# Kernel optimization log

Measured on AMD Instinct MI355X. Metric: run time of the kernel, lower is better.

Reference implementation:

```python
import jax, jax.numpy as jnp
import numpy as np

N, E, F, R = 10000, 320000, 128, 20


def _cross_dim1(a, b):
    # a: [E,3,F], b: [E,3,1]; cross product along axis 1 (broadcast over F)
    return jnp.stack([
        a[:, 1] * b[:, 2] - a[:, 2] * b[:, 1],
        a[:, 2] * b[:, 0] - a[:, 0] * b[:, 2],
        a[:, 0] * b[:, 1] - a[:, 1] * b[:, 0],
    ], axis=1)


def setup_inputs() -> dict:
    key = jax.random.key(0)
    ks = jax.random.split(key, 15)
    s = jax.random.normal(ks[0], (N, F), jnp.float32)
    v = jax.random.normal(ks[1], (N, 3, F), jnp.float32)
    re1 = jax.random.normal(ks[2], (E, R), jnp.float32)
    re2 = jax.random.normal(ks[3], (E, R), jnp.float32)
    f1 = jax.random.uniform(ks[4], (E,), jnp.float32)
    f2 = jax.random.uniform(ks[5], (E,), jnp.float32)
    u1 = jax.random.normal(ks[6], (E, 3), jnp.float32)
    u2 = jax.random.normal(ks[7], (E, 3), jnp.float32)
    edge_index = jax.random.randint(ks[8], (2, E), 0, N, jnp.int32)
    # mlp_phi: Linear(F,F) -> SiLU -> Linear(F,6F); linear_W: Linear(R,6F)
    W1 = jax.random.normal(ks[9], (F, F), jnp.float32) / np.sqrt(F)
    b1 = jnp.zeros((F,), jnp.float32)
    W2 = jax.random.normal(ks[10], (F, 6 * F), jnp.float32) / np.sqrt(F)
    b2 = jnp.zeros((6 * F,), jnp.float32)
    Wr = jax.random.normal(ks[11], (R, 6 * F), jnp.float32) / np.sqrt(R)
    br = jnp.zeros((6 * F,), jnp.float32)
    return dict(s=s, v=v, radial_embeddings_1=re1, radial_embeddings_2=re2,
                f_cut_1=f1, f_cut_2=f2, unit_vectors_1=u1, unit_vectors_2=u2,
                edge_index=edge_index, W1=W1, b1=b1, W2=W2, b2=b2, Wr=Wr, br=br)


def reference(s, v, radial_embeddings_1, radial_embeddings_2, f_cut_1, f_cut_2,
              unit_vectors_1, unit_vectors_2, edge_index, W1, b1, W2, b2, Wr, br):
    idx_i, idx_j = edge_index[0], edge_index[1]
    n_nodes = s.shape[0]
    nf = W1.shape[0]
    # phi: [N, 6F]
    phi = jax.nn.silu(s @ W1 + b1) @ W2 + b2
    # radial gate: [E, 6F]
    W = (radial_embeddings_1 @ Wr + br) * f_cut_1[:, None] \
        + (radial_embeddings_2 @ Wr + br) * f_cut_2[:, None]
    x = phi[idx_j] * W  # [E, 6F]
    x_s, x_vv, x_vs_1, x_vs_2, x_vc_1, x_vc_2 = [
        x[:, i * nf:(i + 1) * nf] for i in range(6)
    ]
    ds = jax.ops.segment_sum(x_s, idx_i, num_segments=n_nodes)  # [N,F]
    v_j = v[idx_j]  # [E,3,F]
    u1 = unit_vectors_1[:, :, None]  # [E,3,1]
    u2 = unit_vectors_2[:, :, None]
    x_v = (v_j * x_vv[:, None, :]
           + x_vs_1[:, None, :] * u1
           + x_vs_2[:, None, :] * u2
           + x_vc_1[:, None, :] * _cross_dim1(v_j, u1)
           + x_vc_2[:, None, :] * _cross_dim1(v_j, u2))  # [E,3,F]
    dv = jax.ops.segment_sum(x_v, idx_i, num_segments=n_nodes)  # [N,3,F]
    return (s + ds, v + dv)
```

## Files before the change

### kernel.cpp

```cpp
#include <hip/hip_runtime.h>
#include <hip/hip_bf16.h>

#define NN   10000
#define NE   320000
#define NF   128
#define SIXF 768
#define K21  21

typedef unsigned short u16;
typedef unsigned int   u32;

__device__ __forceinline__ float bf2f_lo(u32 pk) { return __uint_as_float(pk << 16); }
__device__ __forceinline__ float bf2f_hi(u32 pk) { return __uint_as_float(pk & 0xffff0000u); }
__device__ __forceinline__ u16 f2bf(float f) {
    u32 x = __float_as_uint(f);
    return (u16)((x + 0x7fffu + ((x >> 16) & 1u)) >> 16);
}

__global__ __launch_bounds__(256) void init_out_kernel(
    const float4* __restrict__ s4, const float4* __restrict__ v4, float4* __restrict__ out4)
{
    int i = blockIdx.x * 256 + threadIdx.x;
    if (i < NN * NF / 4) out4[i] = s4[i];
    else                 out4[i] = v4[i - NN * NF / 4];
}

__global__ __launch_bounds__(256) void phi_kernel(
    const float* __restrict__ s, const float* __restrict__ W1, const float* __restrict__ b1,
    const float* __restrict__ W2, const float* __restrict__ b2, u16* __restrict__ phiw)
{
    __shared__ float sh[32][NF];
    __shared__ float hh[32][NF];
    const int t = threadIdx.x;
    const int row0 = blockIdx.x * 32;

    for (int i = t; i < 32 * NF / 4; i += 256) {
        int r = i >> 5, c4 = i & 31;
        float4 val = make_float4(0.f, 0.f, 0.f, 0.f);
        if (row0 + r < NN) val = *reinterpret_cast<const float4*>(&s[(size_t)(row0 + r) * NF + c4 * 4]);
        *reinterpret_cast<float4*>(&sh[r][c4 * 4]) = val;
    }
    __syncthreads();
    {
        const int c = t & 127;
        const int half = t >> 7;
        float hacc[16];
        #pragma unroll
        for (int i = 0; i < 16; ++i) hacc[i] = 0.f;
        for (int k4 = 0; k4 < 32; ++k4) {
            float w0 = W1[(k4 * 4 + 0) * NF + c];
            float w1 = W1[(k4 * 4 + 1) * NF + c];
            float w2 = W1[(k4 * 4 + 2) * NF + c];
            float w3 = W1[(k4 * 4 + 3) * NF + c];
            #pragma unroll
            for (int rr = 0; rr < 16; ++rr) {
                float4 sv = *reinterpret_cast<const float4*>(&sh[half * 16 + rr][k4 * 4]);
                hacc[rr] = fmaf(sv.x, w0, hacc[rr]);
                hacc[rr] = fmaf(sv.y, w1, hacc[rr]);
                hacc[rr] = fmaf(sv.z, w2, hacc[rr]);
                hacc[rr] = fmaf(sv.w, w3, hacc[rr]);
            }
        }
        float b1c = b1[c];
        #pragma unroll
        for (int rr = 0; rr < 16; ++rr) {
            float x = hacc[rr] + b1c;
            float sg = 1.0f / (1.0f + __expf(-x));
            hh[half * 16 + rr][c] = x * sg;
        }
    }
    __syncthreads();
    {
        float pa[32][3];
        #pragma unroll
        for (int r = 0; r < 32; ++r)
            #pragma unroll
            for (int cg = 0; cg < 3; ++cg) pa[r][cg] = 0.f;

        for (int k4 = 0; k4 < 32; ++k4) {
            float w[4][3];
            #pragma unroll
            for (int kk = 0; kk < 4; ++kk)
                #pragma unroll
                for (int cg = 0; cg < 3; ++cg)
                    w[kk][cg] = W2[(size_t)(k4 * 4 + kk) * SIXF + t + 256 * cg];
            #pragma unroll
            for (int r = 0; r < 32; ++r) {
                float4 hv = *reinterpret_cast<const float4*>(&hh[r][k4 * 4]);
                #pragma unroll
                for (int cg = 0; cg < 3; ++cg) {
                    pa[r][cg] = fmaf(hv.x, w[0][cg], pa[r][cg]);
                    pa[r][cg] = fmaf(hv.y, w[1][cg], pa[r][cg]);
                    pa[r][cg] = fmaf(hv.z, w[2][cg], pa[r][cg]);
                    pa[r][cg] = fmaf(hv.w, w[3][cg], pa[r][cg]);
                }
            }
        }
        float b2c[3] = { b2[t], b2[t + 256], b2[t + 512] };
        #pragma unroll
        for (int r = 0; r < 32; ++r) {
            if (row0 + r < NN) {
                #pragma unroll
                for (int cg = 0; cg < 3; ++cg)
                    phiw[(size_t)(row0 + r) * SIXF + t + 256 * cg] = f2bf(pa[r][cg] + b2c[cg]);
            }
        }
    }
}

__global__ __launch_bounds__(256) void prep_wrb_kernel(
    const float* __restrict__ Wr, const float* __restrict__ br, u16* __restrict__ wrb)
{
    int i = blockIdx.x * 256 + threadIdx.x;
    if (i < 21 * SIXF) wrb[i] = f2bf(i < 20 * SIXF ? Wr[i] : br[i - 20 * SIXF]);
}

__global__ __launch_bounds__(256) void prep_vbf_kernel(
    const float* __restrict__ v, u16* __restrict__ vbf)
{
    int i = blockIdx.x * 256 + threadIdx.x;
    if (i < NN * 384) vbf[i] = f2bf(v[i]);
}

__global__ __launch_bounds__(256) void zero_cnt_kernel(int* __restrict__ cnt) {
    int i = blockIdx.x * 256 + threadIdx.x;
    if (i < NN) cnt[i] = 0;
}

__global__ __launch_bounds__(256) void hist_kernel(const int* __restrict__ eidx, int* __restrict__ cnt) {
    int e = blockIdx.x * 256 + threadIdx.x;
    if (e < NE) atomicAdd(&cnt[eidx[e]], 1);
}

__global__ __launch_bounds__(256) void scan_kernel(const int* __restrict__ cnt, int* __restrict__ offs) {
    __shared__ int part[256];
    const int t = threadIdx.x;
    int lsum = 0;
    if (t < 250) {
        #pragma unroll 4
        for (int k = 0; k < 40; ++k) lsum += cnt[t * 40 + k];
    }
    part[t] = lsum;
    __syncthreads();
    if (t == 0) {
        int run = 0;
        for (int i = 0; i < 250; ++i) { int c = part[i]; part[i] = run; run += c; }
    }
    __syncthreads();
    if (t < 250) {
        int run = part[t];
        for (int k = 0; k < 40; ++k) {
            int idx = t * 40 + k;
            offs[idx] = run;
            run += cnt[idx];
        }
    }
}

__global__ __launch_bounds__(256) void scatter_kernel(
    const int* __restrict__ eidx, int* __restrict__ offs, int* __restrict__ elist) {
    int e = blockIdx.x * 256 + threadIdx.x;
    if (e < NE) {
        int pos = atomicAdd(&offs[eidx[e]], 1);
        elist[pos] = e;
    }
}

template<bool USE_VBF>
__global__ __launch_bounds__(256, 4) void gather_kernel(
    const float* __restrict__ re1, const float* __restrict__ re2,
    const float* __restrict__ f1, const float* __restrict__ f2,
    const float* __restrict__ u1v, const float* __restrict__ u2v,
    const int* __restrict__ eidx,
    const u16* __restrict__ phiw, const float* __restrict__ v,
    const u16* __restrict__ vbf, const u16* __restrict__ wrb,
    const float* __restrict__ s,
    const int* __restrict__ cnt, const int* __restrict__ offs,
    const int* __restrict__ elist,
    float* __restrict__ out)
{
    __shared__ u16   WrB[K21][SIXF];
    __shared__ float smem[2048];
    float (*rrs)[K21] = (float(*)[K21])smem;
    float (*euv)[6]   = (float(*)[6])(smem + 672);
    int*   ejd        = (int*)(smem + 864);
    float (*redbuf)[512] = (float(*)[512])smem;

    const int t = threadIdx.x;
    const int node = blockIdx.x;
    const int deg   = cnt[node];
    const int end   = offs[node];
    const int start = end - deg;

    {
        const u32* wg = (const u32*)wrb;
        u32* wl = (u32*)&WrB[0][0];
        for (int i = t; i < 8064; i += 256) wl[i] = wg[i];
    }

    const int wave = t >> 6, lane = t & 63;
    float accS[2] = {0.f, 0.f};
    float accV[3][2] = {{0.f,0.f},{0.f,0.f},{0.f,0.f}};

    for (int base = 0; base < deg; base += 32) {
        const int m = min(32, deg - base);
        __syncthreads();
        for (int i = t; i < m * K21; i += 256) {
            int el = i / K21, r = i - el * K21;
            int e = elist[start + base + el];
            float a;
            if (r < 20) a = f1[e] * re1[(size_t)e * 20 + r] + f2[e] * re2[(size_t)e * 20 + r];
            else        a = f1[e] + f2[e];
            rrs[el][r] = a;
        }
        if (t < m) {
            int e = elist[start + base + t];
            ejd[t] = eidx[NE + e];
            #pragma unroll
            for (int d = 0; d < 3; ++d) {
                euv[t][d]     = u1v[(size_t)e * 3 + d];
                euv[t][3 + d] = u2v[(size_t)e * 3 + d];
            }
        }
        __syncthreads();

        #pragma unroll 1
        for (int half = 0; half < 2; ++half) {
            const int eg = wave * 8 + half * 4;
            if (eg >= m) continue;
            float acc[4][12];
            #pragma unroll
            for (int ea = 0; ea < 4; ++ea)
                #pragma unroll
                for (int cb = 0; cb < 12; ++cb) acc[ea][cb] = 0.f;

            for (int r = 0; r < K21; ++r) {
                float wv[12];
                #pragma unroll
                for (int cc = 0; cc < 6; ++cc) {
                    u32 pk = *reinterpret_cast<const u32*>(&WrB[r][cc * 128 + 2 * lane]);
                    wv[2 * cc]     = bf2f_lo(pk);
                    wv[2 * cc + 1] = bf2f_hi(pk);
                }
                #pragma unroll
                for (int e4 = 0; e4 < 4; ++e4) {
                    float a = rrs[eg + e4][r];
                    #pragma unroll
                    for (int c = 0; c < 12; ++c) acc[e4][c] = fmaf(a, wv[c], acc[e4][c]);
                }
            }

            #pragma unroll
            for (int e4 = 0; e4 < 4; ++e4) {
                const int el = eg + e4;
                if (el < m) {
                    const int nj = ejd[el];
                    const float u1x = euv[el][0], u1y = euv[el][1], u1z = euv[el][2];
                    const float u2x = euv[el][3], u2y = euv[el][4], u2z = euv[el][5];
                    const u16* ph = phiw + (size_t)nj * SIXF + 2 * lane;
                    float px[12];
                    #pragma unroll
                    for (int cc = 0; cc < 6; ++cc) {
                        u32 pk = *reinterpret_cast<const u32*>(ph + cc * 128);
                        px[2 * cc]     = bf2f_lo(pk);
                        px[2 * cc + 1] = bf2f_hi(pk);
                    }
                    float2 va, vb, vc;
                    if (USE_VBF) {
                        const u16* vj = vbf + (size_t)nj * 384 + 2 * lane;
                        u32 p0 = *reinterpret_cast<const u32*>(vj);
                        u32 p1 = *reinterpret_cast<const u32*>(vj + 128);
                        u32 p2 = *reinterpret_cast<const u32*>(vj + 256);
                        va = make_float2(bf2f_lo(p0), bf2f_hi(p0));
                        vb = make_float2(bf2f_lo(p1), bf2f_hi(p1));
                        vc = make_float2(bf2f_lo(p2), bf2f_hi(p2));
                    } else {
                        const float* vj = v + (size_t)nj * 384 + 2 * lane;
                        va = *reinterpret_cast<const float2*>(vj);
                        vb = *reinterpret_cast<const float2*>(vj + 128);
                        vc = *reinterpret_cast<const float2*>(vj + 256);
                    }
                    #pragma unroll
                    for (int ff = 0; ff < 2; ++ff) {
                        float xs   = acc[e4][0 + ff]  * px[0 + ff];
                        float xvv  = acc[e4][2 + ff]  * px[2 + ff];
                        float xvs1 = acc[e4][4 + ff]  * px[4 + ff];
                        float xvs2 = acc[e4][6 + ff]  * px[6 + ff];
                        float xvc1 = acc[e4][8 + ff]  * px[8 + ff];
                        float xvc2 = acc[e4][10 + ff] * px[10 + ff];
                        float a0 = ff ? va.y : va.x;
                        float a1 = ff ? vb.y : vb.x;
                        float a2 = ff ? vc.y : vc.x;
                        float c1x = a1 * u1z - a2 * u1y;
                        float c1y = a2 * u1x - a0 * u1z;
                        float c1z = a0 * u1y - a1 * u1x;
                        float c2x = a1 * u2z - a2 * u2y;
                        float c2y = a2 * u2x - a0 * u2z;
                        float c2z = a0 * u2y - a1 * u2x;
                        accS[ff] += xs;
                        accV[0][ff] += a0 * xvv + xvs1 * u1x + xvs2 * u2x + xvc1 * c1x + xvc2 * c2x;
                        accV[1][ff] += a1 * xvv + xvs1 * u1y + xvs2 * u2y + xvc1 * c1y + xvc2 * c2y;
                        accV[2][ff] += a2 * xvv + xvs1 * u1z + xvs2 * u2z + xvc1 * c1z + xvc2 * c2z;
                    }
                }
            }
        }
    }

    __syncthreads();
    #pragma unroll
    for (int ff = 0; ff < 2; ++ff) {
        redbuf[wave][2 * lane + ff] = accS[ff];
        #pragma unroll
        for (int d = 0; d < 3; ++d)
            redbuf[wave][128 + d * 128 + 2 * lane + ff] = accV[d][ff];
    }
    __syncthreads();
    for (int k = t; k < 512; k += 256) {
        float sum = redbuf[0][k] + redbuf[1][k] + redbuf[2][k] + redbuf[3][k];
        if (k < NF) {
            out[(size_t)node * NF + k] = s[(size_t)node * NF + k] + sum;
        } else {
            int kv = k - NF;
            out[(size_t)NN * NF + (size_t)node * 384 + kv] = v[(size_t)node * 384 + kv] + sum;
        }
    }
}

__global__ __launch_bounds__(256) void edge_kernel(
    const float* __restrict__ re1, const float* __restrict__ re2,
    const float* __restrict__ f1, const float* __restrict__ f2,
    const float* __restrict__ u1v, const float* __restrict__ u2v,
    const int* __restrict__ eidx,
    const u16* __restrict__ phiw, const float* __restrict__ v,
    const float* __restrict__ Wr, const float* __restrict__ br,
    float* __restrict__ out)
{
    __shared__ u16   WrB[K21][SIXF];
    __shared__ float rrs[32][K21];
    __shared__ float euv[32][6];
    __shared__ int   eid[32][2];
    const int t = threadIdx.x;
    const int e0 = blockIdx.x * 32;

    for (int i = t; i < 20 * SIXF; i += 256) WrB[0][i] = f2bf(Wr[i]);
    for (int c = t; c < SIXF; c += 256)      WrB[20][c] = f2bf(br[c]);
    for (int i = t; i < 32 * K21; i += 256) {
        int el = i / K21, r = i - el * K21;
        int e = e0 + el;
        float a;
        if (r < 20) a = f1[e] * re1[(size_t)e * 20 + r] + f2[e] * re2[(size_t)e * 20 + r];
        else        a = f1[e] + f2[e];
        rrs[el][r] = a;
    }
    if (t < 32) {
        int e = e0 + t;
        eid[t][0] = eidx[e];
        eid[t][1] = eidx[NE + e];
        #pragma unroll
        for (int d = 0; d < 3; ++d) {
            euv[t][d]     = u1v[(size_t)e * 3 + d];
            euv[t][3 + d] = u2v[(size_t)e * 3 + d];
        }
    }
    __syncthreads();

    const int wave = t >> 6, lane = t & 63;
    #pragma unroll 1
    for (int half = 0; half < 2; ++half) {
        const int eg = wave * 8 + half * 4;
        float acc[4][12];
        #pragma unroll
        for (int ea = 0; ea < 4; ++ea)
            #pragma unroll
            for (int cb = 0; cb < 12; ++cb) acc[ea][cb] = 0.f;

        for (int r = 0; r < K21; ++r) {
            float wv[12];
            #pragma unroll
            for (int cc = 0; cc < 6; ++cc) {
                u32 pk = *reinterpret_cast<const u32*>(&WrB[r][cc * 128 + 2 * lane]);
                wv[2 * cc]     = bf2f_lo(pk);
                wv[2 * cc + 1] = bf2f_hi(pk);
            }
            #pragma unroll
            for (int e4 = 0; e4 < 4; ++e4) {
                float a = rrs[eg + e4][r];
                #pragma unroll
                for (int c = 0; c < 12; ++c) acc[e4][c] = fmaf(a, wv[c], acc[e4][c]);
            }
        }

        #pragma unroll
        for (int e4 = 0; e4 < 4; ++e4) {
            const int el = eg + e4;
            const int ni = eid[el][0], nj = eid[el][1];
            const float u1x = euv[el][0], u1y = euv[el][1], u1z = euv[el][2];
            const float u2x = euv[el][3], u2y = euv[el][4], u2z = euv[el][5];
            const u16* ph = phiw + (size_t)nj * SIXF + 2 * lane;
            float px[12];
            #pragma unroll
            for (int cc = 0; cc < 6; ++cc) {
                u32 pk = *reinterpret_cast<const u32*>(ph + cc * 128);
                px[2 * cc]     = bf2f_lo(pk);
                px[2 * cc + 1] = bf2f_hi(pk);
            }
            const float* vj = v + (size_t)nj * 384 + 2 * lane;
            float2 va = *reinterpret_cast<const float2*>(vj);
            float2 vb = *reinterpret_cast<const float2*>(vj + 128);
            float2 vc = *reinterpret_cast<const float2*>(vj + 256);
            float* po = out + (size_t)ni * NF + 2 * lane;
            float* pv = out + (size_t)NN * NF + (size_t)ni * 384 + 2 * lane;
            #pragma unroll
            for (int ff = 0; ff < 2; ++ff) {
                float xs   = acc[e4][0 + ff]  * px[0 + ff];
                float xvv  = acc[e4][2 + ff]  * px[2 + ff];
                float xvs1 = acc[e4][4 + ff]  * px[4 + ff];
                float xvs2 = acc[e4][6 + ff]  * px[6 + ff];
                float xvc1 = acc[e4][8 + ff]  * px[8 + ff];
                float xvc2 = acc[e4][10 + ff] * px[10 + ff];
                float a0 = ff ? va.y : va.x;
                float a1 = ff ? vb.y : vb.x;
                float a2 = ff ? vc.y : vc.x;
                float c1x = a1 * u1z - a2 * u1y;
                float c1y = a2 * u1x - a0 * u1z;
                float c1z = a0 * u1y - a1 * u1x;
                float c2x = a1 * u2z - a2 * u2y;
                float c2y = a2 * u2x - a0 * u2z;
                float c2z = a0 * u2y - a1 * u2x;
                float xv0 = a0 * xvv + xvs1 * u1x + xvs2 * u2x + xvc1 * c1x + xvc2 * c2x;
                float xv1 = a1 * xvv + xvs1 * u1y + xvs2 * u2y + xvc1 * c1y + xvc2 * c2y;
                float xv2 = a2 * xvv + xvs1 * u1z + xvs2 * u2z + xvc1 * c1z + xvc2 * c2z;
                unsafeAtomicAdd(po + ff, xs);
                unsafeAtomicAdd(pv + ff, xv0);
                unsafeAtomicAdd(pv + 128 + ff, xv1);
                unsafeAtomicAdd(pv + 256 + ff, xv2);
            }
        }
    }
}

extern "C" void kernel_launch(void* const* d_in, const int* in_sizes, int n_in,
                              void* d_out, int out_size, void* d_ws, size_t ws_size,
                              hipStream_t stream) {
    const float* s   = (const float*)d_in[0];
    const float* v   = (const float*)d_in[1];
    const float* re1 = (const float*)d_in[2];
    const float* re2 = (const float*)d_in[3];
    const float* f1  = (const float*)d_in[4];
    const float* f2  = (const float*)d_in[5];
    const float* u1  = (const float*)d_in[6];
    const float* u2  = (const float*)d_in[7];
    const int*   ei  = (const int*)d_in[8];
    const float* W1  = (const float*)d_in[9];
    const float* b1  = (const float*)d_in[10];
    const float* W2  = (const float*)d_in[11];
    const float* b2  = (const float*)d_in[12];
    const float* Wr  = (const float*)d_in[13];
    const float* br  = (const float*)d_in[14];
    float* out = (float*)d_out;

    const size_t PHI_B  = (size_t)NN * SIXF * 2;
    const size_t VBF_B  = (size_t)NN * 384 * 2;
    const size_t CNT_B  = (size_t)NN * 4;
    const size_t EL_B   = (size_t)NE * 4;
    const size_t WRB_B  = (size_t)21 * SIXF * 2;

    const size_t need_full = PHI_B + VBF_B + 2 * CNT_B + EL_B + WRB_B;
    const size_t need_csr  = PHI_B + 2 * CNT_B + EL_B + WRB_B;

    u16* phiw = (u16*)d_ws;
    phi_kernel<<<dim3((NN + 31) / 32), dim3(256), 0, stream>>>(s, W1, b1, W2, b2, phiw);

    if (ws_size >= need_full) {
        u16* vbf   = (u16*)((char*)d_ws + PHI_B);
        int* cnt   = (int*)((char*)d_ws + PHI_B + VBF_B);
        int* offs  = cnt + NN;
        int* elist = offs + NN;
        u16* wrb   = (u16*)((char*)elist + EL_B);

        prep_wrb_kernel<<<dim3((21 * SIXF + 255) / 256), dim3(256), 0, stream>>>(Wr, br, wrb);
        prep_vbf_kernel<<<dim3((NN * 384 + 255) / 256), dim3(256), 0, stream>>>(v, vbf);
        zero_cnt_kernel<<<dim3((NN + 255) / 256), dim3(256), 0, stream>>>(cnt);
        hist_kernel<<<dim3((NE + 255) / 256), dim3(256), 0, stream>>>(ei, cnt);
        scan_kernel<<<dim3(1), dim3(256), 0, stream>>>(cnt, offs);
        scatter_kernel<<<dim3((NE + 255) / 256), dim3(256), 0, stream>>>(ei, offs, elist);
        gather_kernel<true><<<dim3(NN), dim3(256), 0, stream>>>(
            re1, re2, f1, f2, u1, u2, ei, phiw, v, vbf, wrb, s, cnt, offs, elist, out);
    } else if (ws_size >= need_csr) {
        int* cnt   = (int*)((char*)d_ws + PHI_B);
        int* offs  = cnt + NN;
        int* elist = offs + NN;
        u16* wrb   = (u16*)((char*)elist + EL_B);

        prep_wrb_kernel<<<dim3((21 * SIXF + 255) / 256), dim3(256), 0, stream>>>(Wr, br, wrb);
        zero_cnt_kernel<<<dim3((NN + 255) / 256), dim3(256), 0, stream>>>(cnt);
        hist_kernel<<<dim3((NE + 255) / 256), dim3(256), 0, stream>>>(ei, cnt);
        scan_kernel<<<dim3(1), dim3(256), 0, stream>>>(cnt, offs);
        scatter_kernel<<<dim3((NE + 255) / 256), dim3(256), 0, stream>>>(ei, offs, elist);
        gather_kernel<false><<<dim3(NN), dim3(256), 0, stream>>>(
            re1, re2, f1, f2, u1, u2, ei, phiw, v, (const u16*)nullptr, wrb, s, cnt, offs, elist, out);
    } else {
        init_out_kernel<<<dim3((NN * NF + NN * 3 * NF) / 4 / 256), dim3(256), 0, stream>>>(
            (const float4*)s, (const float4*)v, (float4*)out);
        edge_kernel<<<dim3(NE / 32), dim3(256), 0, stream>>>(
            re1, re2, f1, f2, u1, u2, ei, phiw, v, Wr, br, out);
    }
}
```

Baseline: 539.7 us.

## Process two nodes per gather block, halve phi tile rows, memset counts

The gather kernel now runs 512-thread blocks that each handle two destination nodes, one per 256-thread half. The shared Wr table load is amortized over two nodes and there are half as many blocks, at the cost of both halves looping to the larger degree with shared barriers. The phi kernel tile is cut from 32 to 16 rows per block to get more blocks and lower register pressure. The zero-count kernel is replaced with hipMemsetAsync.

```diff
diff --git a/kernel.cpp b/kernel.cpp
--- a/kernel.cpp
+++ b/kernel.cpp
@@ -29,12 +29,12 @@
     const float* __restrict__ s, const float* __restrict__ W1, const float* __restrict__ b1,
     const float* __restrict__ W2, const float* __restrict__ b2, u16* __restrict__ phiw)
 {
-    __shared__ float sh[32][NF];
-    __shared__ float hh[32][NF];
+    __shared__ float sh[16][NF];
+    __shared__ float hh[16][NF];
     const int t = threadIdx.x;
-    const int row0 = blockIdx.x * 32;
-
-    for (int i = t; i < 32 * NF / 4; i += 256) {
+    const int row0 = blockIdx.x * 16;
+
+    for (int i = t; i < 16 * NF / 4; i += 256) {
         int r = i >> 5, c4 = i & 31;
         float4 val = make_float4(0.f, 0.f, 0.f, 0.f);
         if (row0 + r < NN) val = *reinterpret_cast<const float4*>(&s[(size_t)(row0 + r) * NF + c4 * 4]);
@@ -44,17 +44,17 @@
     {
         const int c = t & 127;
         const int half = t >> 7;
-        float hacc[16];
-        #pragma unroll
-        for (int i = 0; i < 16; ++i) hacc[i] = 0.f;
+        float hacc[8];
+        #pragma unroll
+        for (int i = 0; i < 8; ++i) hacc[i] = 0.f;
         for (int k4 = 0; k4 < 32; ++k4) {
             float w0 = W1[(k4 * 4 + 0) * NF + c];
             float w1 = W1[(k4 * 4 + 1) * NF + c];
             float w2 = W1[(k4 * 4 + 2) * NF + c];
             float w3 = W1[(k4 * 4 + 3) * NF + c];
             #pragma unroll
-            for (int rr = 0; rr < 16; ++rr) {
-                float4 sv = *reinterpret_cast<const float4*>(&sh[half * 16 + rr][k4 * 4]);
+            for (int rr = 0; rr < 8; ++rr) {
+                float4 sv = *reinterpret_cast<const float4*>(&sh[half * 8 + rr][k4 * 4]);
                 hacc[rr] = fmaf(sv.x, w0, hacc[rr]);
                 hacc[rr] = fmaf(sv.y, w1, hacc[rr]);
                 hacc[rr] = fmaf(sv.z, w2, hacc[rr]);
@@ -63,17 +63,17 @@
         }
         float b1c = b1[c];
         #pragma unroll
-        for (int rr = 0; rr < 16; ++rr) {
+        for (int rr = 0; rr < 8; ++rr) {
             float x = hacc[rr] + b1c;
             float sg = 1.0f / (1.0f + __expf(-x));
-            hh[half * 16 + rr][c] = x * sg;
+            hh[half * 8 + rr][c] = x * sg;
         }
     }
     __syncthreads();
     {
-        float pa[32][3];
-        #pragma unroll
-        for (int r = 0; r < 32; ++r)
+        float pa[16][3];
+        #pragma unroll
+        for (int r = 0; r < 16; ++r)
             #pragma unroll
             for (int cg = 0; cg < 3; ++cg) pa[r][cg] = 0.f;
 
@@ -85,7 +85,7 @@
                 for (int cg = 0; cg < 3; ++cg)
                     w[kk][cg] = W2[(size_t)(k4 * 4 + kk) * SIXF + t + 256 * cg];
             #pragma unroll
-            for (int r = 0; r < 32; ++r) {
+            for (int r = 0; r < 16; ++r) {
                 float4 hv = *reinterpret_cast<const float4*>(&hh[r][k4 * 4]);
                 #pragma unroll
                 for (int cg = 0; cg < 3; ++cg) {
@@ -98,7 +98,7 @@
         }
         float b2c[3] = { b2[t], b2[t + 256], b2[t + 512] };
         #pragma unroll
-        for (int r = 0; r < 32; ++r) {
+        for (int r = 0; r < 16; ++r) {
             if (row0 + r < NN) {
                 #pragma unroll
                 for (int cg = 0; cg < 3; ++cg)
@@ -120,11 +120,6 @@
 {
     int i = blockIdx.x * 256 + threadIdx.x;
     if (i < NN * 384) vbf[i] = f2bf(v[i]);
-}
-
-__global__ __launch_bounds__(256) void zero_cnt_kernel(int* __restrict__ cnt) {
-    int i = blockIdx.x * 256 + threadIdx.x;
-    if (i < NN) cnt[i] = 0;
 }
 
 __global__ __launch_bounds__(256) void hist_kernel(const int* __restrict__ eidx, int* __restrict__ cnt) {
@@ -167,7 +162,7 @@
 }
 
 template<bool USE_VBF>
-__global__ __launch_bounds__(256, 4) void gather_kernel(
+__global__ __launch_bounds__(512, 4) void gather_kernel(
     const float* __restrict__ re1, const float* __restrict__ re2,
     const float* __restrict__ f1, const float* __restrict__ f2,
     const float* __restrict__ u1v, const float* __restrict__ u2v,
@@ -180,49 +175,62 @@
     float* __restrict__ out)
 {
     __shared__ u16   WrB[K21][SIXF];
-    __shared__ float smem[2048];
-    float (*rrs)[K21] = (float(*)[K21])smem;
-    float (*euv)[6]   = (float(*)[6])(smem + 672);
-    int*   ejd        = (int*)(smem + 864);
-    float (*redbuf)[512] = (float(*)[512])smem;
-
-    const int t = threadIdx.x;
-    const int node = blockIdx.x;
-    const int deg   = cnt[node];
+    __shared__ float smem[2][1024];
+
+    const int t    = threadIdx.x;
+    const int side = t >> 8;
+    const int tl   = t & 255;
+    const int node = blockIdx.x * 2 + side;
+
+    float (*rrs)[K21] = (float(*)[K21])smem[side];
+    float (*euv)[6]   = (float(*)[6])(smem[side] + 672);
+    int*   ejd        = (int*)(smem[side] + 864);
+    float (*redbuf)[512] = (float(*)[512])smem[side];
+
+    const int degA = cnt[blockIdx.x * 2];
+    const int degB = cnt[blockIdx.x * 2 + 1];
+    const int deg  = side ? degB : degA;
+    const int md   = degA > degB ? degA : degB;
+    const int iters = (md + 31) >> 5;
     const int end   = offs[node];
     const int start = end - deg;
 
     {
         const u32* wg = (const u32*)wrb;
         u32* wl = (u32*)&WrB[0][0];
-        for (int i = t; i < 8064; i += 256) wl[i] = wg[i];
-    }
-
-    const int wave = t >> 6, lane = t & 63;
+        for (int i = t; i < 8064; i += 512) wl[i] = wg[i];
+    }
+
+    const int wave = (t >> 6) & 3;
+    const int lane = t & 63;
     float accS[2] = {0.f, 0.f};
     float accV[3][2] = {{0.f,0.f},{0.f,0.f},{0.f,0.f}};
 
-    for (int base = 0; base < deg; base += 32) {
-        const int m = min(32, deg - base);
+    for (int it = 0; it < iters; ++it) {
+        const int base = it * 32;
+        const int m = deg - base < 32 ? deg - base : 32;
         __syncthreads();
-        for (int i = t; i < m * K21; i += 256) {
-            int el = i / K21, r = i - el * K21;
-            int e = elist[start + base + el];
-            float a;
-            if (r < 20) a = f1[e] * re1[(size_t)e * 20 + r] + f2[e] * re2[(size_t)e * 20 + r];
-            else        a = f1[e] + f2[e];
-            rrs[el][r] = a;
-        }
-        if (t < m) {
-            int e = elist[start + base + t];
-            ejd[t] = eidx[NE + e];
-            #pragma unroll
-            for (int d = 0; d < 3; ++d) {
-                euv[t][d]     = u1v[(size_t)e * 3 + d];
-                euv[t][3 + d] = u2v[(size_t)e * 3 + d];
+        if (m > 0) {
+            for (int i = tl; i < m * K21; i += 256) {
+                int el = i / K21, r = i - el * K21;
+                int e = elist[start + base + el];
+                float a;
+                if (r < 20) a = f1[e] * re1[(size_t)e * 20 + r] + f2[e] * re2[(size_t)e * 20 + r];
+                else        a = f1[e] + f2[e];
+                rrs[el][r] = a;
+            }
+            if (tl < m) {
+                int e = elist[start + base + tl];
+                ejd[tl] = eidx[NE + e];
+                #pragma unroll
+                for (int d = 0; d < 3; ++d) {
+                    euv[tl][d]     = u1v[(size_t)e * 3 + d];
+                    euv[tl][3 + d] = u2v[(size_t)e * 3 + d];
+                }
             }
         }
         __syncthreads();
+        if (m <= 0) continue;
 
         #pragma unroll 1
         for (int half = 0; half < 2; ++half) {
@@ -308,16 +316,28 @@
     }
 
     __syncthreads();
-    #pragma unroll
-    for (int ff = 0; ff < 2; ++ff) {
-        redbuf[wave][2 * lane + ff] = accS[ff];
-        #pragma unroll
-        for (int d = 0; d < 3; ++d)
-            redbuf[wave][128 + d * 128 + 2 * lane + ff] = accV[d][ff];
-    }
-    __syncthreads();
-    for (int k = t; k < 512; k += 256) {
-        float sum = redbuf[0][k] + redbuf[1][k] + redbuf[2][k] + redbuf[3][k];
+    if (wave >= 2) {
+        #pragma unroll
+        for (int ff = 0; ff < 2; ++ff) {
+            redbuf[wave - 2][2 * lane + ff] = accS[ff];
+            #pragma unroll
+            for (int d = 0; d < 3; ++d)
+                redbuf[wave - 2][128 + d * 128 + 2 * lane + ff] = accV[d][ff];
+        }
+    }
+    __syncthreads();
+    if (wave < 2) {
+        #pragma unroll
+        for (int ff = 0; ff < 2; ++ff) {
+            redbuf[wave][2 * lane + ff] += accS[ff];
+            #pragma unroll
+            for (int d = 0; d < 3; ++d)
+                redbuf[wave][128 + d * 128 + 2 * lane + ff] += accV[d][ff];
+        }
+    }
+    __syncthreads();
+    for (int k = tl; k < 512; k += 256) {
+        float sum = redbuf[0][k] + redbuf[1][k];
         if (k < NF) {
             out[(size_t)node * NF + k] = s[(size_t)node * NF + k] + sum;
         } else {
@@ -470,7 +490,7 @@
     const size_t need_csr  = PHI_B + 2 * CNT_B + EL_B + WRB_B;
 
     u16* phiw = (u16*)d_ws;
-    phi_kernel<<<dim3((NN + 31) / 32), dim3(256), 0, stream>>>(s, W1, b1, W2, b2, phiw);
+    phi_kernel<<<dim3((NN + 15) / 16), dim3(256), 0, stream>>>(s, W1, b1, W2, b2, phiw);
 
     if (ws_size >= need_full) {
         u16* vbf   = (u16*)((char*)d_ws + PHI_B);
@@ -481,11 +501,11 @@
 
         prep_wrb_kernel<<<dim3((21 * SIXF + 255) / 256), dim3(256), 0, stream>>>(Wr, br, wrb);
         prep_vbf_kernel<<<dim3((NN * 384 + 255) / 256), dim3(256), 0, stream>>>(v, vbf);
-        zero_cnt_kernel<<<dim3((NN + 255) / 256), dim3(256), 0, stream>>>(cnt);
+        hipMemsetAsync(cnt, 0, CNT_B, stream);
         hist_kernel<<<dim3((NE + 255) / 256), dim3(256), 0, stream>>>(ei, cnt);
         scan_kernel<<<dim3(1), dim3(256), 0, stream>>>(cnt, offs);
         scatter_kernel<<<dim3((NE + 255) / 256), dim3(256), 0, stream>>>(ei, offs, elist);
-        gather_kernel<true><<<dim3(NN), dim3(256), 0, stream>>>(
+        gather_kernel<true><<<dim3(NN / 2), dim3(512), 0, stream>>>(
             re1, re2, f1, f2, u1, u2, ei, phiw, v, vbf, wrb, s, cnt, offs, elist, out);
     } else if (ws_size >= need_csr) {
         int* cnt   = (int*)((char*)d_ws + PHI_B);
@@ -494,11 +514,11 @@
         u16* wrb   = (u16*)((char*)elist + EL_B);
 
         prep_wrb_kernel<<<dim3((21 * SIXF + 255) / 256), dim3(256), 0, stream>>>(Wr, br, wrb);
-        zero_cnt_kernel<<<dim3((NN + 255) / 256), dim3(256), 0, stream>>>(cnt);
+        hipMemsetAsync(cnt, 0, CNT_B, stream);
         hist_kernel<<<dim3((NE + 255) / 256), dim3(256), 0, stream>>>(ei, cnt);
         scan_kernel<<<dim3(1), dim3(256), 0, stream>>>(cnt, offs);
         scatter_kernel<<<dim3((NE + 255) / 256), dim3(256), 0, stream>>>(ei, offs, elist);
-        gather_kernel<false><<<dim3(NN), dim3(256), 0, stream>>>(
+        gather_kernel<false><<<dim3(NN / 2), dim3(512), 0, stream>>>(
             re1, re2, f1, f2, u1, u2, ei, phiw, v, (const u16*)nullptr, wrb, s, cnt, offs, elist, out);
     } else {
         init_out_kernel<<<dim3((NN * NF + NN * 3 * NF) / 4 / 256), dim3(256), 0, stream>>>(
```

After: 573.9 us. 6.4% more time.
